# Kernel optimization log

Hardware: AMD Instinct MI355X
Metric: run time of the kernel (lower is better)

## Reference

```python
import jax, jax.numpy as jnp
import numpy as np

B, N, D_IN, L, H, NB = 4, 512, 32, 64, 128, 2

def setup_inputs() -> dict:
    key = jax.random.key(0)
    ks = jax.random.split(key, 8)
    s = lambda k, shape, fan: jax.random.normal(k, shape, dtype=jnp.float32) / np.float32(np.sqrt(fan))
    return {
        "X": jax.random.normal(ks[0], (B, N, D_IN), dtype=jnp.float32),
        "proj_w": s(ks[1], (D_IN, L), D_IN),
        "proj_b": jnp.zeros((L,), jnp.float32),
        "rn_w1": s(ks[2], (NB, 2 * L, H), 2 * L),
        "rn_b1": jnp.zeros((NB, H), jnp.float32),
        "rn_w2": s(ks[3], (NB, H, L), H),
        "rn_b2": jnp.zeros((NB, L), jnp.float32),
        "fc_w1": s(ks[4], (NB, L, H), L),
        "fc_b1": jnp.zeros((NB, H), jnp.float32),
        "fc_w2": s(ks[5], (NB, H, L), H),
        "fc_b2": jnp.zeros((NB, L), jnp.float32),
        "dec_w": s(ks[6], (L, 1), L),
        "dec_b": jnp.zeros((1,), jnp.float32),
    }

def _rn_block(Z, rw1, rb1, rw2, rb2, fw1, fb1, fw2, fb2):
    # RelationNetwork: pairs[b,n,m] = concat(Y[b,m], X[b,n]) with X=Y=Z.
    # First linear on concat splits into two small GEMMs (Y-half of rw1 first).
    Ldim = Z.shape[-1]
    M = Z.shape[1]
    y_lin = Z @ rw1[:Ldim]          # [B,M,H]  (Y occupies first L cols of pairs)
    x_lin = Z @ rw1[Ldim:]          # [B,N,H]
    h = jax.nn.relu(x_lin[:, :, None, :] + y_lin[:, None, :, :] + rb1)  # [B,N,M,H]
    # sum-pool over M commutes with the second linear layer
    rn_out = h.sum(axis=2) @ rw2 + M * rb2  # [B,N,L]
    Z = Z + rn_out
    Z = Z + (jax.nn.relu(Z @ fw1 + fb1) @ fw2 + fb2)
    return Z

def reference(X, proj_w, proj_b, rn_w1, rn_b1, rn_w2, rn_b2, fc_w1, fc_b1, fc_w2, fc_b2, dec_w, dec_b):
    Z = X @ proj_w + proj_b  # [B,N,L]
    for i in range(rn_w1.shape[0]):  # fixed small num_blocks
        Z = _rn_block(Z, rn_w1[i], rn_b1[i], rn_w2[i], rn_b2[i],
                      fc_w1[i], fc_b1[i], fc_w2[i], fc_b2[i])
    pooled = Z.sum(axis=1)           # pool2='sum' over set dim
    out = pooled @ dec_w + dec_b     # [B,1]
    return out.squeeze(-1)           # [B]
```

## Files before the change

kernel.cpp:

```cpp
#include <hip/hip_runtime.h>

#define B 4
#define N 512
#define DIN 32
#define L 64
#define H 128
#define NB 2
#define R (B * N)

__global__ void k_proj_lin(const float* __restrict__ X, const float* __restrict__ PW,
                           const float* __restrict__ PB, const float* __restrict__ w1,
                           const float* __restrict__ b1, float* __restrict__ Z,
                           float* __restrict__ ylin, float* __restrict__ xlin,
                           float* __restrict__ out) {
    int r = threadIdx.x / 128;
    int t = threadIdx.x % 128;
    int row = blockIdx.x * 2 + r;
    __shared__ float zrow[2][L];

    if (blockIdx.x == 0 && threadIdx.x < B) out[threadIdx.x] = 0.f;

    if (t < L) {
        const float* x = X + row * DIN;
        float acc = PB[t];
#pragma unroll
        for (int k = 0; k < DIN; ++k) acc += x[k] * PW[k * L + t];
        zrow[r][t] = acc;
        Z[row * L + t] = acc;
    }
    __syncthreads();
    float ay = b1[t];
    float ax = 0.f;
#pragma unroll
    for (int k = 0; k < L; ++k) {
        float zv = zrow[r][k];
        ay += zv * w1[k * H + t];
        ax += zv * w1[(L + k) * H + t];
    }
    ylin[row * H + t] = ay;
    xlin[row * H + t] = ax;
}

__global__ void k_pair(const float* __restrict__ xlin, const float* __restrict__ ylin,
                       float* __restrict__ hsum) {
    __shared__ float ycol[N * 32];
    int bid = blockIdx.x;
    int b  = bid >> 7;
    int rem = bid & 127;
    int h0 = (rem >> 5) * 32;
    int n0 = (rem & 31) * 16;
    int t = threadIdx.x;

    const float* ybase = ylin + (size_t)b * N * H + h0;
    for (int i4 = t; i4 < N * 32 / 4; i4 += 256) {
        int m = i4 >> 3;
        int hl0 = (i4 & 7) * 4;
        ((float4*)ycol)[i4] = *(const float4*)(ybase + m * H + hl0);
    }
    __syncthreads();

    int hl = t & 31;
    int h = h0 + hl;
    int na = n0 + (t >> 5) * 2;
    int nb = na + 1;
    float xa = xlin[((size_t)b * N + na) * H + h];
    float xb = xlin[((size_t)b * N + nb) * H + h];
    float aa = 0.f, ab = 0.f;
#pragma unroll 8
    for (int m = 0; m < N; ++m) {
        float y = ycol[m * 32 + hl];
        aa += fmaxf(xa + y, 0.f);
        ab += fmaxf(xb + y, 0.f);
    }
    hsum[((size_t)b * N + na) * H + h] = aa;
    hsum[((size_t)b * N + nb) * H + h] = ab;
}

template <bool FINAL>
__global__ void k_post(const float* __restrict__ hsum, const float* __restrict__ w2,
                       const float* __restrict__ b2, const float* __restrict__ fw1,
                       const float* __restrict__ fb1, const float* __restrict__ fw2,
                       const float* __restrict__ fb2, const float* __restrict__ nw1,
                       const float* __restrict__ nb1, float* __restrict__ Z,
                       float* __restrict__ ylin, float* __restrict__ xlin,
                       const float* __restrict__ dw, const float* __restrict__ db,
                       float* __restrict__ out) {
    __shared__ float wbuf[H * L];
    __shared__ float hl_[8][H];
    __shared__ float zl[8][L];
    __shared__ float tl[8][H];
    __shared__ float part[4];

    int t = threadIdx.x;
    int row0 = blockIdx.x * 8;

    ((float4*)hl_)[t] = ((const float4*)(hsum + (size_t)row0 * H))[t];
    if (t < 128) ((float4*)zl)[t] = ((const float4*)(Z + (size_t)row0 * L))[t];
#pragma unroll
    for (int j = 0; j < 8; ++j)
        ((float4*)wbuf)[t + j * 256] = ((const float4*)w2)[t + j * 256];
    __syncthreads();

    {
        int l = t & 63;
        int r0 = (t >> 6) * 2, r1 = r0 + 1;
        float a0 = 0.f, a1 = 0.f;
#pragma unroll
        for (int kk = 0; kk < H; kk += 4) {
            float4 h0v = *(float4*)&hl_[r0][kk];
            float4 h1v = *(float4*)&hl_[r1][kk];
            float w0 = wbuf[(kk + 0) * L + l];
            float w1v = wbuf[(kk + 1) * L + l];
            float w2v = wbuf[(kk + 2) * L + l];
            float w3 = wbuf[(kk + 3) * L + l];
            a0 += h0v.x * w0 + h0v.y * w1v + h0v.z * w2v + h0v.w * w3;
            a1 += h1v.x * w0 + h1v.y * w1v + h1v.z * w2v + h1v.w * w3;
        }
        float nb2 = (float)N * b2[l];
        zl[r0][l] += a0 + nb2;
        zl[r1][l] += a1 + nb2;
    }
    __syncthreads();
#pragma unroll
    for (int j = 0; j < 8; ++j)
        ((float4*)wbuf)[t + j * 256] = ((const float4*)fw1)[t + j * 256];
    __syncthreads();

    {
        int h = t & 127;
        int rq = (t >> 7) * 4;
        float acc0 = 0.f, acc1 = 0.f, acc2 = 0.f, acc3 = 0.f;
#pragma unroll
        for (int ll = 0; ll < L; ll += 4) {
            float w0 = wbuf[(ll + 0) * H + h];
            float w1v = wbuf[(ll + 1) * H + h];
            float w2v = wbuf[(ll + 2) * H + h];
            float w3 = wbuf[(ll + 3) * H + h];
            float4 z0 = *(float4*)&zl[rq + 0][ll];
            float4 z1 = *(float4*)&zl[rq + 1][ll];
            float4 z2 = *(float4*)&zl[rq + 2][ll];
            float4 z3 = *(float4*)&zl[rq + 3][ll];
            acc0 += z0.x * w0 + z0.y * w1v + z0.z * w2v + z0.w * w3;
            acc1 += z1.x * w0 + z1.y * w1v + z1.z * w2v + z1.w * w3;
            acc2 += z2.x * w0 + z2.y * w1v + z2.z * w2v + z2.w * w3;
            acc3 += z3.x * w0 + z3.y * w1v + z3.z * w2v + z3.w * w3;
        }
        float bb = fb1[h];
        tl[rq + 0][h] = fmaxf(acc0 + bb, 0.f);
        tl[rq + 1][h] = fmaxf(acc1 + bb, 0.f);
        tl[rq + 2][h] = fmaxf(acc2 + bb, 0.f);
        tl[rq + 3][h] = fmaxf(acc3 + bb, 0.f);
    }
    __syncthreads();
#pragma unroll
    for (int j = 0; j < 8; ++j)
        ((float4*)wbuf)[t + j * 256] = ((const float4*)fw2)[t + j * 256];
    __syncthreads();

    float zfin0, zfin1;
    int l_ = t & 63;
    int r0_ = (t >> 6) * 2, r1_ = r0_ + 1;
    {
        float a0 = 0.f, a1 = 0.f;
#pragma unroll
        for (int kk = 0; kk < H; kk += 4) {
            float4 t0v = *(float4*)&tl[r0_][kk];
            float4 t1v = *(float4*)&tl[r1_][kk];
            float w0 = wbuf[(kk + 0) * L + l_];
            float w1v = wbuf[(kk + 1) * L + l_];
            float w2v = wbuf[(kk + 2) * L + l_];
            float w3 = wbuf[(kk + 3) * L + l_];
            a0 += t0v.x * w0 + t0v.y * w1v + t0v.z * w2v + t0v.w * w3;
            a1 += t1v.x * w0 + t1v.y * w1v + t1v.z * w2v + t1v.w * w3;
        }
        float bb = fb2[l_];
        zfin0 = zl[r0_][l_] + a0 + bb;
        zfin1 = zl[r1_][l_] + a1 + bb;
    }

    if (FINAL) {
        float v = (zfin0 + zfin1) * dw[l_];
#pragma unroll
        for (int off = 32; off > 0; off >>= 1) v += __shfl_down(v, off);
        if (l_ == 0) part[t >> 6] = v;
        __syncthreads();
        if (t == 0) {
            float s = part[0] + part[1] + part[2] + part[3];
            if ((row0 % N) == 0) s += db[0];
            atomicAdd(out + row0 / N, s);
        }
        return;
    }

    __syncthreads();
    zl[r0_][l_] = zfin0;
    zl[r1_][l_] = zfin1;
    Z[(size_t)(row0 + r0_) * L + l_] = zfin0;
    Z[(size_t)(row0 + r1_) * L + l_] = zfin1;
    __syncthreads();

#pragma unroll
    for (int j = 0; j < 8; ++j)
        ((float4*)wbuf)[t + j * 256] = ((const float4*)nw1)[t + j * 256];
    __syncthreads();
    {
        int h = t & 127;
        int rq = (t >> 7) * 4;
        float acc0 = nb1[h], acc1 = acc0, acc2 = acc0, acc3 = acc0;
#pragma unroll
        for (int kk = 0; kk < L; kk += 4) {
            float w0 = wbuf[(kk + 0) * H + h];
            float w1v = wbuf[(kk + 1) * H + h];
            float w2v = wbuf[(kk + 2) * H + h];
            float w3 = wbuf[(kk + 3) * H + h];
            float4 z0 = *(float4*)&zl[rq + 0][kk];
            float4 z1 = *(float4*)&zl[rq + 1][kk];
            float4 z2 = *(float4*)&zl[rq + 2][kk];
            float4 z3 = *(float4*)&zl[rq + 3][kk];
            acc0 += z0.x * w0 + z0.y * w1v + z0.z * w2v + z0.w * w3;
            acc1 += z1.x * w0 + z1.y * w1v + z1.z * w2v + z1.w * w3;
            acc2 += z2.x * w0 + z2.y * w1v + z2.z * w2v + z2.w * w3;
            acc3 += z3.x * w0 + z3.y * w1v + z3.z * w2v + z3.w * w3;
        }
        ylin[(size_t)(row0 + rq + 0) * H + h] = acc0;
        ylin[(size_t)(row0 + rq + 1) * H + h] = acc1;
        ylin[(size_t)(row0 + rq + 2) * H + h] = acc2;
        ylin[(size_t)(row0 + rq + 3) * H + h] = acc3;
    }
    __syncthreads();
#pragma unroll
    for (int j = 0; j < 8; ++j)
        ((float4*)wbuf)[t + j * 256] = ((const float4*)(nw1 + L * H))[t + j * 256];
    __syncthreads();
    {
        int h = t & 127;
        int rq = (t >> 7) * 4;
        float acc0 = 0.f, acc1 = 0.f, acc2 = 0.f, acc3 = 0.f;
#pragma unroll
        for (int kk = 0; kk < L; kk += 4) {
            float w0 = wbuf[(kk + 0) * H + h];
            float w1v = wbuf[(kk + 1) * H + h];
            float w2v = wbuf[(kk + 2) * H + h];
            float w3 = wbuf[(kk + 3) * H + h];
            float4 z0 = *(float4*)&zl[rq + 0][kk];
            float4 z1 = *(float4*)&zl[rq + 1][kk];
            float4 z2 = *(float4*)&zl[rq + 2][kk];
            float4 z3 = *(float4*)&zl[rq + 3][kk];
            acc0 += z0.x * w0 + z0.y * w1v + z0.z * w2v + z0.w * w3;
            acc1 += z1.x * w0 + z1.y * w1v + z1.z * w2v + z1.w * w3;
            acc2 += z2.x * w0 + z2.y * w1v + z2.z * w2v + z2.w * w3;
            acc3 += z3.x * w0 + z3.y * w1v + z3.z * w2v + z3.w * w3;
        }
        xlin[(size_t)(row0 + rq + 0) * H + h] = acc0;
        xlin[(size_t)(row0 + rq + 1) * H + h] = acc1;
        xlin[(size_t)(row0 + rq + 2) * H + h] = acc2;
        xlin[(size_t)(row0 + rq + 3) * H + h] = acc3;
    }
}

extern "C" void kernel_launch(void* const* d_in, const int* in_sizes, int n_in,
                              void* d_out, int out_size, void* d_ws, size_t ws_size,
                              hipStream_t stream) {
    const float* X      = (const float*)d_in[0];
    const float* proj_w = (const float*)d_in[1];
    const float* proj_b = (const float*)d_in[2];
    const float* rn_w1  = (const float*)d_in[3];
    const float* rn_b1  = (const float*)d_in[4];
    const float* rn_w2  = (const float*)d_in[5];
    const float* rn_b2  = (const float*)d_in[6];
    const float* fc_w1  = (const float*)d_in[7];
    const float* fc_b1  = (const float*)d_in[8];
    const float* fc_w2  = (const float*)d_in[9];
    const float* fc_b2  = (const float*)d_in[10];
    const float* dec_w  = (const float*)d_in[11];
    const float* dec_b  = (const float*)d_in[12];
    float* out = (float*)d_out;

    float* ws   = (float*)d_ws;
    float* Z    = ws;
    float* ylin = Z + R * L;
    float* xlin = ylin + R * H;
    float* hsum = xlin + R * H;

    k_proj_lin<<<R / 2, 256, 0, stream>>>(X, proj_w, proj_b, rn_w1, rn_b1, Z, ylin, xlin, out);
    k_pair<<<512, 256, 0, stream>>>(xlin, ylin, hsum);
    k_post<false><<<R / 8, 256, 0, stream>>>(hsum, rn_w2, rn_b2, fc_w1, fc_b1, fc_w2, fc_b2,
                                             rn_w1 + 2 * L * H, rn_b1 + H, Z, ylin, xlin,
                                             nullptr, nullptr, nullptr);
    k_pair<<<512, 256, 0, stream>>>(xlin, ylin, hsum);
    k_post<true><<<R / 8, 256, 0, stream>>>(hsum, rn_w2 + H * L, rn_b2 + L,
                                            fc_w1 + L * H, fc_b1 + H, fc_w2 + H * L, fc_b2 + L,
                                            nullptr, nullptr, Z, nullptr, nullptr,
                                            dec_w, dec_b, out);
}
```

Before: 70.25 us.

## Replace quadratic pairwise relu-sum with sort, suffix sums and binary search

The pairwise kernel summed relu(x_n + y_m) over all 512 m for every n and h, which is O(N^2) per column. The new kernel has one block per (batch, hidden) column. It bitonic-sorts the y values in shared memory, builds suffix sums, and for each n binary-searches the count of y > -x. The result is then count*x + suffix_sum, giving O(N log^2 N) work per column. The cost is many __syncthreads barriers in the sort, strided column loads from global memory, and a different floating-point summation order.

```diff
diff --git a/kernel.cpp b/kernel.cpp
--- a/kernel.cpp
+++ b/kernel.cpp
@@ -1,4 +1,5 @@
 #include <hip/hip_runtime.h>
+#include <math.h>
 
 #define B 4
 #define N 512
@@ -41,39 +42,70 @@
     xlin[row * H + t] = ax;
 }
 
-__global__ void k_pair(const float* __restrict__ xlin, const float* __restrict__ ylin,
-                       float* __restrict__ hsum) {
-    __shared__ float ycol[N * 32];
-    int bid = blockIdx.x;
-    int b  = bid >> 7;
-    int rem = bid & 127;
-    int h0 = (rem >> 5) * 32;
-    int n0 = (rem & 31) * 16;
+__global__ void k_pairsort(const float* __restrict__ xlin, const float* __restrict__ ylin,
+                           float* __restrict__ hsum) {
+    __shared__ float ys[1024];
+    __shared__ float ss[N + 1];
+    __shared__ float csum[64];
+    __shared__ float csuf[65];
+
     int t = threadIdx.x;
-
-    const float* ybase = ylin + (size_t)b * N * H + h0;
-    for (int i4 = t; i4 < N * 32 / 4; i4 += 256) {
-        int m = i4 >> 3;
-        int hl0 = (i4 & 7) * 4;
-        ((float4*)ycol)[i4] = *(const float4*)(ybase + m * H + hl0);
-    }
-    __syncthreads();
-
-    int hl = t & 31;
-    int h = h0 + hl;
-    int na = n0 + (t >> 5) * 2;
-    int nb = na + 1;
-    float xa = xlin[((size_t)b * N + na) * H + h];
-    float xb = xlin[((size_t)b * N + nb) * H + h];
-    float aa = 0.f, ab = 0.f;
-#pragma unroll 8
-    for (int m = 0; m < N; ++m) {
-        float y = ycol[m * 32 + hl];
-        aa += fmaxf(xa + y, 0.f);
-        ab += fmaxf(xb + y, 0.f);
-    }
-    hsum[((size_t)b * N + na) * H + h] = aa;
-    hsum[((size_t)b * N + nb) * H + h] = ab;
+    int b = blockIdx.x >> 7;
+    int h = blockIdx.x & 127;
+
+    const float* ycol = ylin + (size_t)b * N * H + h;
+    for (int m = t; m < N; m += 256) ys[m] = ycol[(size_t)m * H];
+    for (int m = N + t; m < 1024; m += 256) ys[m] = INFINITY;
+    __syncthreads();
+
+    for (int k = 2; k <= N; k <<= 1) {
+        for (int j = k >> 1; j > 0; j >>= 1) {
+            int i = ((t & ~(j - 1)) << 1) | (t & (j - 1));
+            int p = i | j;
+            float a = ys[i], c = ys[p];
+            bool up = (i & k) == 0;
+            if ((a > c) == up) { ys[i] = c; ys[p] = a; }
+            __syncthreads();
+        }
+    }
+
+    if (t < 64) {
+        float s = 0.f;
+        int base = t * 8;
+#pragma unroll
+        for (int q = 7; q >= 0; --q) s += ys[base + q];
+        csum[t] = s;
+    }
+    __syncthreads();
+    if (t == 0) {
+        csuf[64] = 0.f;
+        float run = 0.f;
+        for (int c = 63; c >= 0; --c) { run += csum[c]; csuf[c] = run; }
+    }
+    __syncthreads();
+    for (int i = t; i < N; i += 256) {
+        float s = csuf[(i >> 3) + 1];
+        int e = i | 7;
+        for (int q = e; q >= i; --q) s += ys[q];
+        ss[i] = s;
+    }
+    if (t == 0) ss[N] = 0.f;
+    __syncthreads();
+
+    const float* xcol = xlin + (size_t)b * N * H + h;
+    float* ocol = hsum + (size_t)b * N * H + h;
+    int n0 = t, n1 = t + 256;
+    float x0 = xcol[(size_t)n0 * H];
+    float x1 = xcol[(size_t)n1 * H];
+    float v0 = -x0, v1 = -x1;
+    int p0 = 0, p1 = 0;
+#pragma unroll
+    for (int s = 512; s >= 1; s >>= 1) {
+        if (ys[p0 + s - 1] <= v0) p0 += s;
+        if (ys[p1 + s - 1] <= v1) p1 += s;
+    }
+    ocol[(size_t)n0 * H] = (float)(N - p0) * x0 + ss[p0];
+    ocol[(size_t)n1 * H] = (float)(N - p1) * x1 + ss[p1];
 }
 
 template <bool FINAL>
@@ -283,11 +315,11 @@
     float* hsum = xlin + R * H;
 
     k_proj_lin<<<R / 2, 256, 0, stream>>>(X, proj_w, proj_b, rn_w1, rn_b1, Z, ylin, xlin, out);
-    k_pair<<<512, 256, 0, stream>>>(xlin, ylin, hsum);
+    k_pairsort<<<B * H, 256, 0, stream>>>(xlin, ylin, hsum);
     k_post<false><<<R / 8, 256, 0, stream>>>(hsum, rn_w2, rn_b2, fc_w1, fc_b1, fc_w2, fc_b2,
                                              rn_w1 + 2 * L * H, rn_b1 + H, Z, ylin, xlin,
                                              nullptr, nullptr, nullptr);
-    k_pair<<<512, 256, 0, stream>>>(xlin, ylin, hsum);
+    k_pairsort<<<B * H, 256, 0, stream>>>(xlin, ylin, hsum);
     k_post<true><<<R / 8, 256, 0, stream>>>(hsum, rn_w2 + H * L, rn_b2 + L,
                                             fc_w1 + L * H, fc_b1 + H, fc_w2 + H * L, fc_b2 + L,
                                             nullptr, nullptr, Z, nullptr, nullptr,
```

New measurement: 60.11 us. 14.4% less time.
